# Kernel optimization log

Hardware: AMD Instinct MI355X
Metric: run time of the kernel (lower is better)

Reference implementation:

```python
import jax, jax.numpy as jnp
import numpy as np

N, T, DM = 8192, 32, 128   # nodes, patches, d_model (d_in = T*DM = 4096)
M, NNZ = 1024, 131072      # hyperedges, incidences
EPS = 1e-5
SLOPE = 0.2


def _bn(x, g, b, axes):
    # BatchNorm with batch statistics (training-mode math, eval dropout)
    m = jnp.mean(x, axis=axes, keepdims=True)
    v = jnp.var(x, axis=axes, keepdims=True)
    return (x - m) / jnp.sqrt(v + EPS) * g + b


def _hconv(x, he_attr, he_n, he_e, W, att, bias, heads):
    # PyG HypergraphConv, use_attention=True, attention_mode='node', concat=False
    out = W.shape[1] // heads
    xt = (x @ W).reshape(N, heads, out)          # [N, H, F]
    et = (he_attr @ W).reshape(M, heads, out)    # [M, H, F]
    xi = xt[he_n]                                # [nnz, H, F] gather node feats
    ej = et[he_e]                                # [nnz, H, F] gather edge feats
    alpha = jnp.sum(jnp.concatenate([xi, ej], axis=-1) * att, axis=-1)  # [nnz, H]
    alpha = jax.nn.leaky_relu(alpha, SLOPE)
    # segment softmax grouped by hyperedge (attention_mode='node')
    amax = jax.ops.segment_max(alpha, he_e, num_segments=M)
    ex = jnp.exp(alpha - amax[he_e])
    alpha = ex / jax.ops.segment_sum(ex, he_e, num_segments=M)[he_e]
    # degree normalizers (hyperedge_weight == 1)
    ones = jnp.ones((NNZ,), x.dtype)
    Dn = jax.ops.segment_sum(ones, he_n, num_segments=N)
    Dinv = jnp.where(Dn > 0, 1.0 / Dn, 0.0)
    Bm = jax.ops.segment_sum(ones, he_e, num_segments=M)
    Binv = jnp.where(Bm > 0, 1.0 / Bm, 0.0)
    # node -> edge, then edge -> node message passing
    eo = jax.ops.segment_sum(alpha[:, :, None] * Binv[he_e][:, None, None] * xi,
                             he_e, num_segments=M)                     # [M, H, F]
    no = jax.ops.segment_sum(alpha[:, :, None] * Dinv[he_n][:, None, None] * eo[he_e],
                             he_n, num_segments=N)                     # [N, H, F]
    return no.mean(axis=1) + bias  # concat=False -> mean over heads


def setup_inputs() -> dict:
    key = jax.random.key(0)
    ks = jax.random.split(key, 16)
    d_in = T * DM
    s = 0.02
    inp = {
        "x": jax.random.normal(ks[0], (N, T, DM), jnp.float32),
        "he_nodes": jax.random.randint(ks[1], (NNZ,), 0, N),
        "he_edges": jax.random.randint(ks[2], (NNZ,), 0, M),
        "W1": jax.random.normal(ks[3], (d_in, DM), jnp.float32) * s,
        "b1": jnp.zeros((DM,), jnp.float32),
        "g1": jnp.ones((DM,), jnp.float32), "be1": jnp.zeros((DM,), jnp.float32),
        "Wh1": jax.random.normal(ks[4], (DM, 4 * DM), jnp.float32) * s,
        "att1": jax.random.normal(ks[5], (1, 4, 2 * DM), jnp.float32) * s,
        "bh1": jnp.zeros((DM,), jnp.float32),
        "g2": jnp.ones((DM,), jnp.float32), "be2": jnp.zeros((DM,), jnp.float32),
        "Wh2": jax.random.normal(ks[6], (DM, DM), jnp.float32) * s,
        "att2": jax.random.normal(ks[7], (1, 1, 2 * DM), jnp.float32) * s,
        "bh2": jnp.zeros((DM,), jnp.float32),
        "g3": jnp.ones((DM,), jnp.float32), "be3": jnp.zeros((DM,), jnp.float32),
        "W3": jax.random.normal(ks[8], (DM, d_in), jnp.float32) * s,
        "b3": jnp.zeros((d_in,), jnp.float32),
        "g4": jnp.ones((DM,), jnp.float32), "be4": jnp.zeros((DM,), jnp.float32),
    }
    return inp


def reference(x, he_nodes, he_edges, W1, b1, g1, be1, Wh1, att1, bh1,
              g2, be2, Wh2, att2, bh2, g3, be3, W3, b3, g4, be4):
    src = x
    h = x.reshape(N, T * DM)
    h = jax.nn.leaky_relu(h @ W1 + b1, SLOPE)
    h = _bn(h, g1, be1, 0)
    # hyperedge_attr = incidence^T @ h  (== to_dense_adj(...).T @ h)
    he_attr = jax.ops.segment_sum(h[he_nodes], he_edges, num_segments=M)
    h = h + _hconv(h, he_attr, he_nodes, he_edges, Wh1, att1, bh1, 4)
    h = _bn(h, g2, be2, 0)
    he_attr = jax.ops.segment_sum(h[he_nodes], he_edges, num_segments=M)
    h = h + _hconv(h, he_attr, he_nodes, he_edges, Wh2, att2, bh2, 1)
    h = _bn(h, g3, be3, 0)
    h = jax.nn.leaky_relu(h @ W3 + b3, SLOPE)
    h = src + h.reshape(N, T, DM)
    h = _bn(h, g4, be4, (0, 1))  # BN over channel DM, stats over (N, T)
    return h
```

## Files before the change

kernel.cpp:

```cpp
#include <hip/hip_runtime.h>
#include <hip/hip_bf16.h>
#include <math.h>

#define NN   8192
#define TT   32
#define DIN  4096
#define MME  1024
#define NNZK 131072
#define EPSV 1e-5f
#define MALL (NN + MME)
#define NSLOT 8

typedef __attribute__((ext_vector_type(8))) short bf16x8;
typedef __attribute__((ext_vector_type(4))) float f32x4;

__device__ __forceinline__ float lrelu(float v){ return v > 0.f ? v : 0.2f*v; }
__device__ __forceinline__ short f2b(float f){
    union { __hip_bfloat16 h; short s; } u; u.h = __float2bfloat16(f); return u.s;
}
__device__ __forceinline__ float b2f(short s){
    union { float f; unsigned u; } u; u.u = ((unsigned)(unsigned short)s) << 16; return u.f;
}

__global__ void zero_i(int* p, int n){ int i = blockIdx.x*256 + threadIdx.x; if (i < n) p[i] = 0; }
__global__ void zero_f(float* p, int n){ int i = blockIdx.x*256 + threadIdx.x; if (i < n) p[i] = 0.f; }

__global__ void count_seg(const int* __restrict__ he_n, const int* __restrict__ he_e,
                          int* __restrict__ ncnt, int* __restrict__ ecnt){
    int k = blockIdx.x*256 + threadIdx.x;
    if (k < NNZK){ atomicAdd(&ecnt[he_e[k]], 1); atomicAdd(&ncnt[he_n[k]], 1); }
}

__device__ void scan_body(const int* __restrict__ cnt, int* __restrict__ off,
                          int* __restrict__ cur, int n){
    int t = threadIdx.x;
    int lane = t & 63, wv = t >> 6;
    int chunk = n >> 10;
    int base = t*chunk;
    int s = 0;
#pragma unroll 4
    for (int i = 0; i < chunk; i++) s += cnt[base+i];
    int v = s;
    for (int d = 1; d < 64; d <<= 1){
        int u = __shfl_up(v, d);
        if (lane >= d) v += u;
    }
    __shared__ int wsum[16];
    if (lane == 63) wsum[wv] = v;
    __syncthreads();
    if (wv == 0 && lane < 16){
        int w2 = wsum[lane];
        for (int d = 1; d < 16; d <<= 1){
            int u = __shfl_up(w2, d);
            if (lane >= d) w2 += u;
        }
        wsum[lane] = w2;
    }
    __syncthreads();
    int excl = v - s + (wv > 0 ? wsum[wv-1] : 0);
    for (int i = 0; i < chunk; i++){
        off[base+i] = excl;
        cur[base+i] = excl;
        excl += cnt[base+i];
    }
    if (t == 1023) off[n] = excl;
}

__global__ void scan2(const int* ecnt, int* eoffb, int* ecur,
                      const int* ncnt, int* noffb, int* ncur){
    if (blockIdx.x == 0) scan_body(ecnt, eoffb, ecur, MME);
    else                 scan_body(ncnt, noffb, ncur, NN);
}

__global__ void fill_both(const int* __restrict__ he_n, const int* __restrict__ he_e,
                          int* __restrict__ ecur, int* __restrict__ ncur,
                          int* __restrict__ eperm, int* __restrict__ enode,
                          int* __restrict__ nperm, int* __restrict__ nedge){
    int k = blockIdx.x*256 + threadIdx.x;
    if (k < NNZK){
        int e = he_e[k], n = he_n[k];
        int p = atomicAdd(&ecur[e], 1); eperm[p] = k; enode[p] = n;
        int q = atomicAdd(&ncur[n], 1); nperm[q] = k; nedge[q] = e;
    }
}

__global__ __launch_bounds__(256) void convert_x(const float4* __restrict__ x,
                                                 bf16x8* __restrict__ xb, int n8){
    int stride = gridDim.x*256;
    for (int i = blockIdx.x*256 + threadIdx.x; i < n8; i += stride){
        float4 lo = x[2*i], hi = x[2*i+1];
        bf16x8 v;
        v[0]=f2b(lo.x); v[1]=f2b(lo.y); v[2]=f2b(lo.z); v[3]=f2b(lo.w);
        v[4]=f2b(hi.x); v[5]=f2b(hi.y); v[6]=f2b(hi.z); v[7]=f2b(hi.w);
        xb[i] = v;
    }
}

__device__ void wconv_body(const float* __restrict__ W, __hip_bfloat16* __restrict__ BT,
                           int K, int N, int gx, int gy){
    __shared__ float tile[32][33];
    int k0 = gy*32, n0 = gx*32;
    int tx = threadIdx.x & 31, ty = threadIdx.x >> 5;
    for (int i = ty; i < 32; i += 8) tile[i][tx] = W[(size_t)(k0+i)*N + n0+tx];
    __syncthreads();
    for (int i = ty; i < 32; i += 8)
        BT[(size_t)(n0+i)*K + k0 + tx] = __float2bfloat16(tile[tx][i]);
}

__global__ void wconv_all(const float* W1, __hip_bfloat16* W1T,
                          const float* Wh1, __hip_bfloat16* Wh1T,
                          const float* Wh2, __hip_bfloat16* Wh2T,
                          const float* W3, __hip_bfloat16* W3T){
    int b = blockIdx.x;
    if (b < 512)            wconv_body(W1,  W1T,  DIN, 128, b % 4,          b / 4);
    else if (b < 576){ b -= 512; wconv_body(Wh1, Wh1T, 128, 512, b % 16, b / 16); }
    else if (b < 592){ b -= 576; wconv_body(Wh2, Wh2T, 128, 128, b % 4,  b / 4); }
    else             { b -= 592; wconv_body(W3,  W3T,  128, DIN, b % 128, b / 128); }
}

#define SWZ(b) ((b) ^ ((((b) >> 6) & 7) << 4))

__global__ __launch_bounds__(256) void gemm_bb(
    const __hip_bfloat16* __restrict__ Ab, const __hip_bfloat16* __restrict__ Bwt,
    __hip_bfloat16* __restrict__ Cb, int M, int N, int K, int kchunk)
{
    __shared__ f32x4 WsRaw[512];
    __shared__ f32x4 XsRaw[512];
    char* Ws = (char*)WsRaw;
    char* Xs = (char*)XsRaw;
    const int tid = threadIdx.x;
    const int lane = tid & 63;
    const int w = tid >> 6;
    const int m0 = blockIdx.y << 7, n0 = blockIdx.x << 7;
    const int kz = blockIdx.z * kchunk;
    const int wN = (w >> 1) << 6, wM = (w & 1) << 6;

    const int s0 = tid, s1 = tid + 256;
    const int r0 = s0 >> 2, k0b = (s0 & 3) << 3;
    const int r1 = s1 >> 2, k1b = (s1 & 3) << 3;
    const __hip_bfloat16* pA0 = Ab + (size_t)(m0 + r0)*K + kz + k0b;
    const __hip_bfloat16* pA1 = Ab + (size_t)(m0 + r1)*K + kz + k1b;
    const __hip_bfloat16* pW0 = Bwt + (size_t)(n0 + r0)*K + kz + k0b;
    const __hip_bfloat16* pW1 = Bwt + (size_t)(n0 + r1)*K + kz + k1b;
    const int wo0 = SWZ(s0 << 4), wo1 = SWZ(s1 << 4);

    int rwOff[4], rxOff[4];
#pragma unroll
    for (int f = 0; f < 4; f++){
        rwOff[f] = SWZ((wN + f*16 + (lane & 15))*64 + ((lane >> 4) << 4));
        rxOff[f] = SWZ((wM + f*16 + (lane & 15))*64 + ((lane >> 4) << 4));
// ... 121 lines not shown
    const int ncb = wN + ((lane >> 4) << 2);
    if (tid < 128) sAx[tid] = 0.f;
    __syncthreads();
    const int h = blockIdx.x;
    const int aoff = (m0 >= NN) ? 128 : 0;
    const float* av = attv + h*256 + aoff;
    float4 a4[4];
#pragma unroll
    for (int i = 0; i < 4; i++) a4[i] = *(const float4*)&av[ncb + i*16];
    float sj[4] = {0.f, 0.f, 0.f, 0.f};
#pragma unroll
    for (int j = 0; j < 4; j++){
        int row = m0 + mc + j*16;
#pragma unroll
        for (int i = 0; i < 4; i++){
            int col = n0 + ncb + i*16;
            f32x4 v = acc[i][j];
            short4 sv = { f2b(v[0]), f2b(v[1]), f2b(v[2]), f2b(v[3]) };
            *(short4*)&Cb[(size_t)row*N + col] = sv;
            sj[j] += v[0]*a4[i].x + v[1]*a4[i].y + v[2]*a4[i].z + v[3]*a4[i].w;
        }
    }
#pragma unroll
    for (int j = 0; j < 4; j++) atomicAdd(&sAx[mc + j*16], sj[j]);
    __syncthreads();
    if (tid < 128){
        int row = m0 + tid;
        float val = sAx[tid];
        if (row < NN) axo[row*H + h] = val;
        else          aeo[(row - NN)*H + h] = val;
    }
}

__global__ __launch_bounds__(256) void gemm_nt7(
    const float* __restrict__ Aact, const __hip_bfloat16* __restrict__ Bwt,
    __hip_bfloat16* __restrict__ Cb, const float* __restrict__ bias,
    const float* __restrict__ coefA, int M, int N, int K)
{
    __shared__ f32x4 WsRaw[512];
    __shared__ f32x4 XsRaw[512];
    char* Ws = (char*)WsRaw;
    char* Xs = (char*)XsRaw;
    const int tid = threadIdx.x;
    const int lane = tid & 63;
    const int w = tid >> 6;
    const int m0 = blockIdx.y << 7, n0 = blockIdx.x << 7;
    const int wN = (w >> 1) << 6, wM = (w & 1) << 6;

    const int s0 = tid, s1 = tid + 256;
    const int r0 = s0 >> 2, k0b = (s0 & 3) << 3;
    const int r1 = s1 >> 2, k1b = (s1 & 3) << 3;
    const float* pX0 = Aact + (size_t)(m0 + r0)*K + k0b;
    const float* pX1 = Aact + (size_t)(m0 + r1)*K + k1b;
    const __hip_bfloat16* pW0 = Bwt + (size_t)(n0 + r0)*K + k0b;
    const __hip_bfloat16* pW1 = Bwt + (size_t)(n0 + r1)*K + k1b;
    const int wo0 = SWZ(s0 << 4), wo1 = SWZ(s1 << 4);

    int rwOff[4], rxOff[4];
#pragma unroll
    for (int f = 0; f < 4; f++){
        rwOff[f] = SWZ((wN + f*16 + (lane & 15))*64 + ((lane >> 4) << 4));
        rxOff[f] = SWZ((wM + f*16 + (lane & 15))*64 + ((lane >> 4) << 4));
    }

    f32x4 acc[4][4] = {};

    float4 x0l = *(const float4*)pX0, x0h = *(const float4*)(pX0+4);
    float4 x1l = *(const float4*)pX1, x1h = *(const float4*)(pX1+4);
    bf16x8 w0 = *(const bf16x8*)pW0, w1 = *(const bf16x8*)pW1;

// ... 22 lines not shown
        *(bf16x8*)(Xs + wo1) = vx1;
        *(bf16x8*)(Ws + wo0) = w0;
        *(bf16x8*)(Ws + wo1) = w1;
        __syncthreads();
        if (ks + 1 < nsteps){
            pX0 += 32; pX1 += 32; pW0 += 32; pW1 += 32;
            x0l = *(const float4*)pX0; x0h = *(const float4*)(pX0+4);
            x1l = *(const float4*)pX1; x1h = *(const float4*)(pX1+4);
            w0 = *(const bf16x8*)pW0;  w1 = *(const bf16x8*)pW1;
        }
        bf16x8 wf[4], xf[4];
#pragma unroll
        for (int f = 0; f < 4; f++){
            wf[f] = *(const bf16x8*)(Ws + rwOff[f]);
            xf[f] = *(const bf16x8*)(Xs + rxOff[f]);
        }
#pragma unroll
        for (int i = 0; i < 4; i++)
#pragma unroll
            for (int j = 0; j < 4; j++)
                acc[i][j] = __builtin_amdgcn_mfma_f32_16x16x32_bf16(wf[i], xf[j], acc[i][j], 0, 0, 0);
    }

    const int mc = wM + (lane & 15);
    const int ncb = wN + ((lane >> 4) << 2);
#pragma unroll
    for (int j = 0; j < 4; j++){
        int row = m0 + mc + j*16;
#pragma unroll
        for (int i = 0; i < 4; i++){
            int col = n0 + ncb + i*16;
            f32x4 v = acc[i][j];
            float4 b4 = *(const float4*)&bias[col];
            short4 sv = { f2b(lrelu(v[0] + b4.x)), f2b(lrelu(v[1] + b4.y)),
                          f2b(lrelu(v[2] + b4.z)), f2b(lrelu(v[3] + b4.w)) };
            *(short4*)&Cb[(size_t)row*N + col] = sv;
        }
    }
}

__global__ void reduce8s(const __hip_bfloat16* __restrict__ part, const float* __restrict__ bias,
                         float* __restrict__ out, int nf4, int parts, float* __restrict__ slots){
    int tid = threadIdx.x;
    int i = blockIdx.x*256 + tid;
    const short4* p4 = (const short4*)part;
    short4 v0 = p4[i];
    float4 s = { b2f(v0.x), b2f(v0.y), b2f(v0.z), b2f(v0.w) };
    for (int z = 1; z < parts; z++){
        short4 p = p4[(size_t)z*nf4 + i];
        s.x += b2f(p.x); s.y += b2f(p.y); s.z += b2f(p.z); s.w += b2f(p.w);
    }
    int c0 = (i & 31) << 2;
    s.x = lrelu(s.x + bias[c0+0]); s.y = lrelu(s.y + bias[c0+1]);
    s.z = lrelu(s.z + bias[c0+2]); s.w = lrelu(s.w + bias[c0+3]);
    ((float4*)out)[i] = s;
    __shared__ float S[128], Q[128];
    if (tid < 128){ S[tid] = 0.f; Q[tid] = 0.f; }
    __syncthreads();
    atomicAdd(&S[c0+0], s.x); atomicAdd(&Q[c0+0], s.x*s.x);
    atomicAdd(&S[c0+1], s.y); atomicAdd(&Q[c0+1], s.y*s.y);
    atomicAdd(&S[c0+2], s.z); atomicAdd(&Q[c0+2], s.z*s.z);
    atomicAdd(&S[c0+3], s.w); atomicAdd(&Q[c0+3], s.w*s.w);
    __syncthreads();
    if (tid < 128){
        int slot = blockIdx.x & (NSLOT-1);
        atomicAdd(&slots[slot*256 + tid], S[tid]);
        atomicAdd(&slots[slot*256 + 128 + tid], Q[tid]);
    }
}

__global__ __launch_bounds__(256) void final_stats(
    const bf16x8* __restrict__ xb, const bf16x8* __restrict__ f,
    float* __restrict__ slots, int n8)
{
    int tid = threadIdx.x;
    float s[8] = {0,0,0,0,0,0,0,0}, q[8] = {0,0,0,0,0,0,0,0};
    int stride = gridDim.x*256;
    for (int i = blockIdx.x*256 + tid; i < n8; i += stride){
        bf16x8 xv = xb[i], fv = f[i];
#pragma unroll
        for (int j = 0; j < 8; j++){
            float y = b2f(xv[j]) + b2f(fv[j]);
            s[j] += y; q[j] += y*y;
        }
    }
    __shared__ float S[128], Q[128];
    if (tid < 128){ S[tid] = 0.f; Q[tid] = 0.f; }
    __syncthreads();
    int c0 = (tid & 15) << 3;
#pragma unroll
    for (int j = 0; j < 8; j++){
        atomicAdd(&S[c0+j], s[j]);
        atomicAdd(&Q[c0+j], q[j]);
    }
    __syncthreads();
    if (tid < 128){
        int slot = blockIdx.x & (NSLOT-1);
        atomicAdd(&slots[slot*256 + tid], S[tid]);
        atomicAdd(&slots[slot*256 + 128 + tid], Q[tid]);
    }
}

__global__ __launch_bounds__(256) void final_apply(
    const bf16x8* __restrict__ xb, const bf16x8* __restrict__ f,
    const float* __restrict__ coef, float4* __restrict__ out, int n8)
{
    int tid = threadIdx.x;
    int c0 = (tid & 15) << 3;
    float sc[8], sh[8];
#pragma unroll
    for (int j = 0; j < 8; j++){ sc[j] = coef[c0+j]; sh[j] = coef[128+c0+j]; }
    int stride = gridDim.x*256;
    for (int i = blockIdx.x*256 + tid; i < n8; i += stride){
        bf16x8 xv = xb[i], fv = f[i];
        float4 lo, hi;
        lo.x = (b2f(xv[0]) + b2f(fv[0]))*sc[0] + sh[0];
        lo.y = (b2f(xv[1]) + b2f(fv[1]))*sc[1] + sh[1];
        lo.z = (b2f(xv[2]) + b2f(fv[2]))*sc[2] + sh[2];
        lo.w = (b2f(xv[3]) + b2f(fv[3]))*sc[3] + sh[3];
        hi.x = (b2f(xv[4]) + b2f(fv[4]))*sc[4] + sh[4];
        hi.y = (b2f(xv[5]) + b2f(fv[5]))*sc[5] + sh[5];
        hi.z = (b2f(xv[6]) + b2f(fv[6]))*sc[6] + sh[6];
        hi.w = (b2f(xv[7]) + b2f(fv[7]))*sc[7] + sh[7];
        out[2*i]   = lo;
        out[2*i+1] = hi;
    }
}

__global__ void bn_stats_v2(const float* __restrict__ x, float* __restrict__ slots, int rows){
    int cg = threadIdx.x & 31, rg = threadIdx.x >> 5;
    float4 s = {0,0,0,0}, q = {0,0,0,0};
    for (int r = blockIdx.x*8 + rg; r < rows; r += gridDim.x*8){
        float4 v = ((const float4*)x)[(size_t)r*32 + cg];
        s.x += v.x; q.x += v.x*v.x;
        s.y += v.y; q.y += v.y*v.y;
        s.z += v.z; q.z += v.z*v.z;
        s.w += v.w; q.w += v.w*v.w;
    }
    __shared__ float S[128], Q[128];
    if (threadIdx.x < 128){ S[threadIdx.x] = 0.f; Q[threadIdx.x] = 0.f; }
    __syncthreads();
    int c0 = cg << 2;
    atomicAdd(&S[c0+0], s.x); atomicAdd(&Q[c0+0], q.x);
    atomicAdd(&S[c0+1], s.y); atomicAdd(&Q[c0+1], q.y);
    atomicAdd(&S[c0+2], s.z); atomicAdd(&Q[c0+2], q.z);
    atomicAdd(&S[c0+3], s.w); atomicAdd(&Q[c0+3], q.w);
    __syncthreads();
    if (threadIdx.x < 128){
        int slot = blockIdx.x & (NSLOT-1);
        atomicAdd(&slots[slot*256 + threadIdx.x], S[threadIdx.x]);
        atomicAdd(&slots[slot*256 + 128 + threadIdx.x], Q[threadIdx.x]);
    }
}

__global__ void bn_finalize2z(float* __restrict__ slots, int nslots,
                              const float* __restrict__ g, const float* __restrict__ b,
                              float invR, float* __restrict__ coef){
    int c = threadIdx.x;
    float s = 0.f, q = 0.f;
    for (int k = 0; k < nslots; k++){
        s += slots[k*256 + c]; q += slots[k*256 + 128 + c];
        slots[k*256 + c] = 0.f; slots[k*256 + 128 + c] = 0.f;
    }
    float m = s*invR;
    float v = q*invR - m*m;
    float sc = g[c]*rsqrtf(v + EPSV);
    coef[c] = sc;
    coef[128 + c] = b[c] - m*sc;
}

__global__ void bn_apply4(float4* __restrict__ x, const float* __restrict__ coef, size_t n4){
    size_t i = (size_t)blockIdx.x*blockDim.x + threadIdx.x;
    size_t stride = (size_t)gridDim.x*blockDim.x;
    for (; i < n4; i += stride){
        int c0 = (int)(i & 31) * 4;
        float4 v = x[i];
        v.x = v.x*coef[c0+0] + coef[128+c0+0];
        v.y = v.y*coef[c0+1] + coef[128+c0+1];
        v.z = v.z*coef[c0+2] + coef[128+c0+2];
        v.w = v.w*coef[c0+3] + coef[128+c0+3];
        x[i] = v;
    }
}

__global__ void seg_sum_edge(const int* __restrict__ eoff, const int* __restrict__ enode,
                             const float* __restrict__ h, float* __restrict__ out){
    int m = blockIdx.x, t = threadIdx.x;
    int jg = t >> 5, cq = t & 31;
    int s0 = eoff[m], cnt = eoff[m+1] - s0;
    __shared__ int sn[128];
    __shared__ float4 comb[4][32];
    float4 acc = {0,0,0,0};
    for (int base = 0; base < cnt; base += 128){
        int i = base + t;
        if (i < cnt) sn[t] = enode[s0+i];
        __syncthreads();
        int lim = min(128, cnt - base);
        for (int j = jg; j < lim; j += 4){
            float4 v = *(const float4*)&h[(size_t)sn[j]*128 + cq*4];
            acc.x += v.x; acc.y += v.y; acc.z += v.z; acc.w += v.w;
        }
        __syncthreads();
    }
    comb[jg][cq] = acc;
    __syncthreads();
    if (t < 32){
        float4 a = comb[0][t], b = comb[1][t], c = comb[2][t], d = comb[3][t];
        float4 tot = { a.x+b.x+c.x+d.x, a.y+b.y+c.y+d.y, a.z+b.z+c.z+d.z, a.w+b.w+c.w+d.w };
        *(float4*)&out[(size_t)m*128 + t*4] = tot;
    }
}

template<int H>
__global__ void seg_softmax(const int* __restrict__ eoff, const int* __restrict__ eperm,
                            const int* __restrict__ enode,
                            const float* __restrict__ ax, const float* __restrict__ ae,
                            float* __restrict__ alpha){
    int m = blockIdx.x, t = threadIdx.x;
    int s0 = eoff[m], cnt = eoff[m+1] - s0;
    if (cnt == 0) return;
    __shared__ float red[128];
    float aeh[H];
#pragma unroll
    for (int h = 0; h < H; h++) aeh[h] = ae[m*H + h];
    float lmax[H];
#pragma unroll
    for (int h = 0; h < H; h++) lmax[h] = -1e30f;
    for (int i = t; i < cnt; i += 128){
        int k = eperm[s0+i]; int n = enode[s0+i];
#pragma unroll
        for (int h = 0; h < H; h++){
            float v = lrelu(ax[n*H + h] + aeh[h]);
            alpha[(size_t)k*H + h] = v;
            lmax[h] = fmaxf(lmax[h], v);
        }
    }
    float gmax[H];
#pragma unroll
    for (int h = 0; h < H; h++){
        red[t] = lmax[h]; __syncthreads();
        for (int s = 64; s > 0; s >>= 1){ if (t < s) red[t] = fmaxf(red[t], red[t+s]); __syncthreads(); }
        gmax[h] = red[0]; __syncthreads();
    }
    float lsum[H];
#pragma unroll
    for (int h = 0; h < H; h++) lsum[h] = 0.f;
    for (int i = t; i < cnt; i += 128){
        int k = eperm[s0+i];
#pragma unroll
        for (int h = 0; h < H; h++){
            float ex = __expf(alpha[(size_t)k*H + h] - gmax[h]);
            alpha[(size_t)k*H + h] = ex;
            lsum[h] += ex;
        }
    }
    float ginv[H];
#pragma unroll
    for (int h = 0; h < H; h++){
        red[t] = lsum[h]; __syncthreads();
        for (int s = 64; s > 0; s >>= 1){ if (t < s) red[t] += red[t+s]; __syncthreads(); }
        ginv[h] = 1.f/red[0]; __syncthreads();
    }
    for (int i = t; i < cnt; i += 128){
        int k = eperm[s0+i];
#pragma unroll
        for (int h = 0; h < H; h++) alpha[(size_t)k*H + h] *= ginv[h];
    }
}

__global__ void seg_eo4(const int* __restrict__ eoff, const int* __restrict__ eperm,
                        const int* __restrict__ enode,
                        const float* __restrict__ alpha, const __hip_bfloat16* __restrict__ xt,
                        float* __restrict__ eo){
    int m = blockIdx.x, t = threadIdx.x;
    int jpar = t >> 7, cq = t & 127;
    int hq = cq >> 5;
    int s0 = eoff[m], cnt = eoff[m+1] - s0;
    __shared__ int sn[128];
    __shared__ float sa[128][4];
    __shared__ float comb[256][4];
    float acc[4] = {0.f, 0.f, 0.f, 0.f};
    for (int base = 0; base < cnt; base += 128){
        int i = base + t;
        if (t < 128 && i < cnt){
            sn[t] = enode[s0+i];
            *(float4*)sa[t] = *(const float4*)&alpha[(size_t)eperm[s0+i]*4];
        }
        __syncthreads();
        int lim = min(128, cnt - base);
        for (int j = jpar; j < lim; j += 2){
            const ushort* p = (const ushort*)xt + (size_t)sn[j]*512 + cq*4;
            ushort4 u = *(const ushort4*)p;
            float a = sa[j][hq];
            acc[0] += a*b2f((short)u.x); acc[1] += a*b2f((short)u.y);
            acc[2] += a*b2f((short)u.z); acc[3] += a*b2f((short)u.w);
        }
        __syncthreads();
    }
    comb[t][0] = acc[0]; comb[t][1] = acc[1]; comb[t][2] = acc[2]; comb[t][3] = acc[3];
    __syncthreads();
    if (t < 128){
        float binv = cnt > 0 ? 1.f/(float)cnt : 0.f;
#pragma unroll
        for (int i2 = 0; i2 < 4; i2++){
            int ch = t*4 + i2;
            int h = ch >> 7, c = ch & 127;
            eo[(size_t)m*512 + c*4 + h] = (comb[t][i2] + comb[t+128][i2]) * binv;
        }
    }
}

__global__ void seg_eo1b(const int* __restrict__ eoff, const int* __restrict__ eperm,
                         const int* __restrict__ enode,
                         const float* __restrict__ alpha, const __hip_bfloat16* __restrict__ xt,
                         float* __restrict__ eo){
    int m = blockIdx.x, t = threadIdx.x;
    int jg = t >> 5, cq = t & 31;
    int s0 = eoff[m], cnt = eoff[m+1] - s0;
    __shared__ int sn[128];
    __shared__ float sa[128];
    __shared__ float4 comb[4][32];
    float4 acc = {0,0,0,0};
    for (int base = 0; base < cnt; base += 128){
        int i = base + t;
        if (i < cnt){
            sn[t] = enode[s0+i];
            sa[t] = alpha[eperm[s0+i]];
        }
        __syncthreads();
        int lim = min(128, cnt - base);
        for (int j = jg; j < lim; j += 4){
            const ushort* p = (const ushort*)xt + (size_t)sn[j]*128 + cq*4;
            ushort4 u = *(const ushort4*)p;
            float a = sa[j];
            acc.x += a*b2f((short)u.x); acc.y += a*b2f((short)u.y);
            acc.z += a*b2f((short)u.z); acc.w += a*b2f((short)u.w);
        }
        __syncthreads();
    }
    comb[jg][cq] = acc;
    __syncthreads();
    if (t < 32){
        float binv = cnt > 0 ? 1.f/(float)cnt : 0.f;
        float4 a = comb[0][t], b = comb[1][t], c = comb[2][t], d = comb[3][t];
        float4 tot = { (a.x+b.x+c.x+d.x)*binv, (a.y+b.y+c.y+d.y)*binv,
                       (a.z+b.z+c.z+d.z)*binv, (a.w+b.w+c.w+d.w)*binv };
        *(float4*)&eo[(size_t)m*128 + t*4] = tot;
    }
}

__global__ void seg_node_out4(const int* __restrict__ noff, const int* __restrict__ nperm,
                              const int* __restrict__ nedge,
                              const float* __restrict__ alpha, const float* __restrict__ eo,
                              const float* __restrict__ hin, const float* __restrict__ bias,
                              float* __restrict__ hout){
    int n = blockIdx.x, c = threadIdx.x;
    int s0 = noff[n], cnt = noff[n+1] - s0;
    float acc = 0.f;
    for (int i = 0; i < cnt; i++){
        int k = nperm[s0+i]; int e = nedge[s0+i];
        float4 al = *(const float4*)&alpha[(size_t)k*4];
        float4 ev = *(const float4*)&eo[(size_t)e*512 + c*4];
        acc += al.x*ev.x + al.y*ev.y + al.z*ev.z + al.w*ev.w;
    }
    float dinv = cnt > 0 ? 1.f/((float)cnt*4.f) : 0.f;
    hout[(size_t)n*128 + c] = hin[(size_t)n*128 + c] + bias[c] + acc*dinv;
}

__global__ void seg_node_out1(const int* __restrict__ noff, const int* __restrict__ nperm,
                              const int* __restrict__ nedge,
                              const float* __restrict__ alpha, const float* __restrict__ eo,
                              const float* __restrict__ hin, const float* __restrict__ bias,
                              float* __restrict__ hout){
    int n = blockIdx.x, c = threadIdx.x;
    int s0 = noff[n], cnt = noff[n+1] - s0;
    float acc = 0.f;
// ... 6 lines not shown
}

extern "C" void kernel_launch(void* const* d_in, const int* in_sizes, int n_in,
                              void* d_out, int out_size, void* d_ws, size_t ws_size,
                              hipStream_t stream){
    const float* x    = (const float*)d_in[0];
    const int*   he_n = (const int*)  d_in[1];
    const int*   he_e = (const int*)  d_in[2];
    const float* W1   = (const float*)d_in[3];
    const float* b1   = (const float*)d_in[4];
    const float* g1   = (const float*)d_in[5];
    const float* be1  = (const float*)d_in[6];
    const float* Wh1  = (const float*)d_in[7];
    const float* att1 = (const float*)d_in[8];
    const float* bh1  = (const float*)d_in[9];
    const float* g2   = (const float*)d_in[10];
    const float* be2  = (const float*)d_in[11];
    const float* Wh2  = (const float*)d_in[12];
    const float* att2 = (const float*)d_in[13];
    const float* bh2  = (const float*)d_in[14];
    const float* g3   = (const float*)d_in[15];
    const float* be3  = (const float*)d_in[16];
    const float* W3   = (const float*)d_in[17];
    const float* b3   = (const float*)d_in[18];
    const float* g4   = (const float*)d_in[19];
    const float* be4  = (const float*)d_in[20];
    float* out = (float*)d_out;

    char* ws = (char*)d_ws;
    size_t off = 0;
    auto alloc = [&](size_t bytes)->char*{ char* p = ws + off; off += (bytes + 255) & ~(size_t)255; return p; };

    char* big = alloc((size_t)NN*DIN*2);
    __hip_bfloat16* fbuf = (__hip_bfloat16*)big;
    __hip_bfloat16* part = (__hip_bfloat16*)big;
    __hip_bfloat16* xt1b = (__hip_bfloat16*)(big + (size_t)16*NN*128*2);
    __hip_bfloat16* xbuf = (__hip_bfloat16*)alloc((size_t)NN*DIN*2);

    float* hall1  = (float*)alloc((size_t)MALL*128*4);
    float* hall2  = (float*)alloc((size_t)MALL*128*4);
    float* h3     = (float*)alloc((size_t)NN*128*4);
    __hip_bfloat16* xt2b = (__hip_bfloat16*)alloc((size_t)MALL*128*2);
    float* eo     = (float*)alloc((size_t)MME*512*4);
    float* alpha  = (float*)alloc((size_t)NNZK*4*4);
    float* ax     = (float*)alloc((size_t)NN*4*4);
    float* ae     = (float*)alloc((size_t)MME*4*4);
    float* slots  = (float*)alloc((size_t)NSLOT*256*4);
    float* coef   = (float*)alloc(256*4);
    __hip_bfloat16* W1T  = (__hip_bfloat16*)alloc((size_t)128*DIN*2);
    __hip_bfloat16* Wh1T = (__hip_bfloat16*)alloc((size_t)512*128*2);
    __hip_bfloat16* Wh2T = (__hip_bfloat16*)alloc((size_t)128*128*2);
    __hip_bfloat16* W3T  = (__hip_bfloat16*)alloc((size_t)DIN*128*2);
    int* ecnt  = (int*)alloc(MME*4);
    int* ncnt  = (int*)alloc(NN*4);
    int* eoffb = (int*)alloc((MME+1)*4);
    int* ecur  = (int*)alloc(MME*4);
    int* noffb = (int*)alloc((NN+1)*4);
    int* ncur  = (int*)alloc(NN*4);
    int* eperm = (int*)alloc((size_t)NNZK*4);
    int* nperm = (int*)alloc((size_t)NNZK*4);
    int* enode = (int*)alloc((size_t)NNZK*4);
    int* nedge = (int*)alloc((size_t)NNZK*4);

    convert_x<<<2048, 256, 0, stream>>>((const float4*)x, (bf16x8*)xbuf, NN*DIN/8);

    zero_i<<<(MME+NN+255)/256, 256, 0, stream>>>(ecnt, MME+NN);
    count_seg<<<NNZK/256, 256, 0, stream>>>(he_n, he_e, ncnt, ecnt);
    scan2<<<2, 1024, 0, stream>>>(ecnt, eoffb, ecur, ncnt, noffb, ncur);
    fill_both<<<NNZK/256, 256, 0, stream>>>(he_n, he_e, ecur, ncur, eperm, enode, nperm, nedge);

    wconv_all<<<1104, 256, 0, stream>>>(W1, W1T, Wh1, Wh1T, Wh2, Wh2T, W3, W3T);

    gemm_bb<<<dim3(1, NN/128, 16), 256, 0, stream>>>(xbuf, W1T, part, NN, 128, DIN, DIN/16);
    zero_f<<<NSLOT, 256, 0, stream>>>(slots, NSLOT*256);
    reduce8s<<<NN*128/4/256, 256, 0, stream>>>(part, b1, hall1, NN*128/4, 16, slots);
    bn_finalize2z<<<1, 128, 0, stream>>>(slots, NSLOT, g1, be1, 1.f/NN, coef);
    bn_apply4<<<1024, 256, 0, stream>>>((float4*)hall1, coef, (size_t)NN*32);

    seg_sum_edge<<<MME, 128, 0, stream>>>(eoffb, enode, hall1, hall1 + (size_t)NN*128);
    gemm_att<4><<<dim3(4, MALL/128), 256, 0, stream>>>(hall1, Wh1T, xt1b, att1, ax, ae, MALL, 512, 128);
    seg_softmax<4><<<MME, 128, 0, stream>>>(eoffb, eperm, enode, ax, ae, alpha);
    seg_eo4<<<MME, 256, 0, stream>>>(eoffb, eperm, enode, alpha, xt1b, eo);
    seg_node_out4<<<NN, 128, 0, stream>>>(noffb, nperm, nedge, alpha, eo, hall1, bh1, hall2);
    bn_stats_v2<<<256, 256, 0, stream>>>(hall2, slots, NN);
    bn_finalize2z<<<1, 128, 0, stream>>>(slots, NSLOT, g2, be2, 1.f/NN, coef);
    bn_apply4<<<1024, 256, 0, stream>>>((float4*)hall2, coef, (size_t)NN*32);

    seg_sum_edge<<<MME, 128, 0, stream>>>(eoffb, enode, hall2, hall2 + (size_t)NN*128);
    gemm_att<1><<<dim3(1, MALL/128), 256, 0, stream>>>(hall2, Wh2T, xt2b, att2, ax, ae, MALL, 128, 128);
    seg_softmax<1><<<MME, 128, 0, stream>>>(eoffb, eperm, enode, ax, ae, alpha);
    seg_eo1b<<<MME, 128, 0, stream>>>(eoffb, eperm, enode, alpha, xt2b, eo);
    seg_node_out1<<<NN, 128, 0, stream>>>(noffb, nperm, nedge, alpha, eo, hall2, bh2, h3);

    bn_stats_v2<<<256, 256, 0, stream>>>(h3, slots, NN);
    bn_finalize2z<<<1, 128, 0, stream>>>(slots, NSLOT, g3, be3, 1.f/NN, coef);

    gemm_nt7<<<dim3(DIN/128, NN/128), 256, 0, stream>>>(h3, W3T, fbuf, b3, coef, NN, DIN, 128);
    final_stats<<<2048, 256, 0, stream>>>((const bf16x8*)xbuf, (const bf16x8*)fbuf, slots, NN*DIN/8);
    bn_finalize2z<<<1, 128, 0, stream>>>(slots, NSLOT, g4, be4, 1.f/((float)NN*TT), coef);
    final_apply<<<2048, 256, 0, stream>>>((const bf16x8*)xbuf, (const bf16x8*)fbuf, coef, (float4*)out, NN*DIN/8);
}
```

Before: 490.0 us.

## Fuse setup kernels, BN finalize tails, softmax+edge aggregation, and residual into GEMM

Merges the x conversion, segment counting and weight transposes into one setup kernel, and merges all zeroing into one kernel. BatchNorm finalization now runs in the last block to arrive, using a ticket counter, which removes separate single-block launches. Segment softmax is fused with the edge aggregation. The residual add is folded into the final GEMM epilogue, so the last stats and apply passes read one bf16 tensor instead of two. The trade-offs are extra atomics and fences, and the residual sum is now rounded to bf16 before the stats are taken.

```diff
diff --git a/kernel.cpp b/kernel.cpp
--- a/kernel.cpp
+++ b/kernel.cpp
@@ -22,13 +22,43 @@
     union { float f; unsigned u; } u; u.u = ((unsigned)(unsigned short)s) << 16; return u.f;
 }
 
-__global__ void zero_i(int* p, int n){ int i = blockIdx.x*256 + threadIdx.x; if (i < n) p[i] = 0; }
-__global__ void zero_f(float* p, int n){ int i = blockIdx.x*256 + threadIdx.x; if (i < n) p[i] = 0.f; }
-
-__global__ void count_seg(const int* __restrict__ he_n, const int* __restrict__ he_e,
-                          int* __restrict__ ncnt, int* __restrict__ ecnt){
-    int k = blockIdx.x*256 + threadIdx.x;
-    if (k < NNZK){ atomicAdd(&ecnt[he_e[k]], 1); atomicAdd(&ncnt[he_n[k]], 1); }
+__global__ void zero_all(int* __restrict__ cnt, int n1, float* __restrict__ slots, int n2,
+                         int* __restrict__ tick, int n3){
+    int i = blockIdx.x*256 + threadIdx.x;
+    if (i < n1) cnt[i] = 0;
+    int j = i - n1;
+    if (j >= 0 && j < n2) slots[j] = 0.f;
+    int k = j - n2;
+    if (k >= 0 && k < n3) tick[k] = 0;
+}
+
+__device__ void finalize_tail(float* __restrict__ slots, int* __restrict__ ticket, int nblocks,
+                              const float* __restrict__ g, const float* __restrict__ b,
+                              float invR, float* __restrict__ coef){
+    __shared__ int isLast;
+    __threadfence();
+    if (threadIdx.x == 0){
+        int old = atomicAdd(ticket, 1);
+        isLast = (old == nblocks - 1) ? 1 : 0;
+    }
+    __syncthreads();
+    if (isLast){
+        __threadfence();
+        if (threadIdx.x < 128){
+            int c = threadIdx.x;
+            float s = 0.f, q = 0.f;
+            for (int k = 0; k < NSLOT; k++){
+                s += slots[k*256 + c]; q += slots[k*256 + 128 + c];
+                slots[k*256 + c] = 0.f; slots[k*256 + 128 + c] = 0.f;
+            }
+            float m = s*invR;
+            float v = q*invR - m*m;
+            float sc = g[c]*rsqrtf(v + EPSV);
+            coef[c] = sc;
+            coef[128 + c] = b[c] - m*sc;
+            if (c == 0) *ticket = 0;
+        }
+    }
 }
 
 __device__ void scan_body(const int* __restrict__ cnt, int* __restrict__ off,
@@ -84,18 +114,6 @@
     }
 }
 
-__global__ __launch_bounds__(256) void convert_x(const float4* __restrict__ x,
-                                                 bf16x8* __restrict__ xb, int n8){
-    int stride = gridDim.x*256;
-    for (int i = blockIdx.x*256 + threadIdx.x; i < n8; i += stride){
-        float4 lo = x[2*i], hi = x[2*i+1];
-        bf16x8 v;
-        v[0]=f2b(lo.x); v[1]=f2b(lo.y); v[2]=f2b(lo.z); v[3]=f2b(lo.w);
-        v[4]=f2b(hi.x); v[5]=f2b(hi.y); v[6]=f2b(hi.z); v[7]=f2b(hi.w);
-        xb[i] = v;
-    }
-}
-
 __device__ void wconv_body(const float* __restrict__ W, __hip_bfloat16* __restrict__ BT,
                            int K, int N, int gx, int gy){
     __shared__ float tile[32][33];
@@ -107,15 +125,33 @@
         BT[(size_t)(n0+i)*K + k0 + tx] = __float2bfloat16(tile[tx][i]);
 }
 
-__global__ void wconv_all(const float* W1, __hip_bfloat16* W1T,
-                          const float* Wh1, __hip_bfloat16* Wh1T,
-                          const float* Wh2, __hip_bfloat16* Wh2T,
-                          const float* W3, __hip_bfloat16* W3T){
+__global__ __launch_bounds__(256) void setup_all(
+    const float4* __restrict__ x, bf16x8* __restrict__ xb,
+    const int* __restrict__ he_n, const int* __restrict__ he_e,
+    int* __restrict__ ncnt, int* __restrict__ ecnt,
+    const float* W1, __hip_bfloat16* W1T, const float* Wh1, __hip_bfloat16* Wh1T,
+    const float* Wh2, __hip_bfloat16* Wh2T, const float* W3, __hip_bfloat16* W3T)
+{
     int b = blockIdx.x;
-    if (b < 512)            wconv_body(W1,  W1T,  DIN, 128, b % 4,          b / 4);
-    else if (b < 576){ b -= 512; wconv_body(Wh1, Wh1T, 128, 512, b % 16, b / 16); }
-    else if (b < 592){ b -= 576; wconv_body(Wh2, Wh2T, 128, 128, b % 4,  b / 4); }
-    else             { b -= 592; wconv_body(W3,  W3T,  128, DIN, b % 128, b / 128); }
+    if (b < 2048){
+        const int n8 = NN*DIN/8;
+        for (int i = b*256 + threadIdx.x; i < n8; i += 2048*256){
+            float4 lo = x[2*i], hi = x[2*i+1];
+            bf16x8 v;
+            v[0]=f2b(lo.x); v[1]=f2b(lo.y); v[2]=f2b(lo.z); v[3]=f2b(lo.w);
+            v[4]=f2b(hi.x); v[5]=f2b(hi.y); v[6]=f2b(hi.z); v[7]=f2b(hi.w);
+            xb[i] = v;
+        }
+    } else if (b < 2560){
+        int k = (b - 2048)*256 + threadIdx.x;
+        if (k < NNZK){ atomicAdd(&ecnt[he_e[k]], 1); atomicAdd(&ncnt[he_n[k]], 1); }
+    } else {
+        int c = b - 2560;
+        if (c < 512)            wconv_body(W1,  W1T,  DIN, 128, c % 4,   c / 4);
+        else if (c < 576){ c -= 512; wconv_body(Wh1, Wh1T, 128, 512, c % 16, c / 16); }
+        else if (c < 592){ c -= 576; wconv_body(Wh2, Wh2T, 128, 128, c % 4,  c / 4); }
+        else             { c -= 592; wconv_body(W3,  W3T,  128, DIN, c % 128, c / 128); }
+    }
 }
 
 #define SWZ(b) ((b) ^ ((((b) >> 6) & 7) << 4))
@@ -303,10 +339,10 @@
     }
 }
 
-__global__ __launch_bounds__(256) void gemm_nt7(
+__global__ __launch_bounds__(256) void gemm_nt8(
     const float* __restrict__ Aact, const __hip_bfloat16* __restrict__ Bwt,
-    __hip_bfloat16* __restrict__ Cb, const float* __restrict__ bias,
-    const float* __restrict__ coefA, int M, int N, int K)
+    const __hip_bfloat16* __restrict__ xb, __hip_bfloat16* __restrict__ Yb,
+    const float* __restrict__ bias, const float* __restrict__ coefA, int M, int N, int K)
 {
     __shared__ f32x4 WsRaw[512];
     __shared__ f32x4 XsRaw[512];
@@ -395,15 +431,20 @@
             int col = n0 + ncb + i*16;
             f32x4 v = acc[i][j];
             float4 b4 = *(const float4*)&bias[col];
-            short4 sv = { f2b(lrelu(v[0] + b4.x)), f2b(lrelu(v[1] + b4.y)),
-                          f2b(lrelu(v[2] + b4.z)), f2b(lrelu(v[3] + b4.w)) };
-            *(short4*)&Cb[(size_t)row*N + col] = sv;
-        }
-    }
-}
-
-__global__ void reduce8s(const __hip_bfloat16* __restrict__ part, const float* __restrict__ bias,
-                         float* __restrict__ out, int nf4, int parts, float* __restrict__ slots){
+            short4 xv = *(const short4*)&xb[(size_t)row*N + col];
+            short4 sv = { f2b(lrelu(v[0] + b4.x) + b2f(xv.x)),
+                          f2b(lrelu(v[1] + b4.y) + b2f(xv.y)),
+                          f2b(lrelu(v[2] + b4.z) + b2f(xv.z)),
+                          f2b(lrelu(v[3] + b4.w) + b2f(xv.w)) };
+            *(short4*)&Yb[(size_t)row*N + col] = sv;
+        }
+    }
+}
+
+__global__ void reduce8s_f(const __hip_bfloat16* __restrict__ part, const float* __restrict__ bias,
+                           float* __restrict__ out, int nf4, int parts, float* __restrict__ slots,
+                           int* __restrict__ ticket, const float* __restrict__ g,
+                           const float* __restrict__ b, float invR, float* __restrict__ coef){
     int tid = threadIdx.x;
     int i = blockIdx.x*256 + tid;
     const short4* p4 = (const short4*)part;
@@ -430,67 +471,12 @@
         atomicAdd(&slots[slot*256 + tid], S[tid]);
         atomicAdd(&slots[slot*256 + 128 + tid], Q[tid]);
     }
-}
-
-__global__ __launch_bounds__(256) void final_stats(
-    const bf16x8* __restrict__ xb, const bf16x8* __restrict__ f,
-    float* __restrict__ slots, int n8)
-{
-    int tid = threadIdx.x;
-    float s[8] = {0,0,0,0,0,0,0,0}, q[8] = {0,0,0,0,0,0,0,0};
-    int stride = gridDim.x*256;
-    for (int i = blockIdx.x*256 + tid; i < n8; i += stride){
-        bf16x8 xv = xb[i], fv = f[i];
-#pragma unroll
-        for (int j = 0; j < 8; j++){
-            float y = b2f(xv[j]) + b2f(fv[j]);
-            s[j] += y; q[j] += y*y;
-        }
-    }
-    __shared__ float S[128], Q[128];
-    if (tid < 128){ S[tid] = 0.f; Q[tid] = 0.f; }
-    __syncthreads();
-    int c0 = (tid & 15) << 3;
-#pragma unroll
-    for (int j = 0; j < 8; j++){
-        atomicAdd(&S[c0+j], s[j]);
-        atomicAdd(&Q[c0+j], q[j]);
-    }
-    __syncthreads();
-    if (tid < 128){
-        int slot = blockIdx.x & (NSLOT-1);
-        atomicAdd(&slots[slot*256 + tid], S[tid]);
-        atomicAdd(&slots[slot*256 + 128 + tid], Q[tid]);
-    }
-}
-
-__global__ __launch_bounds__(256) void final_apply(
-    const bf16x8* __restrict__ xb, const bf16x8* __restrict__ f,
-    const float* __restrict__ coef, float4* __restrict__ out, int n8)
-{
-    int tid = threadIdx.x;
-    int c0 = (tid & 15) << 3;
-    float sc[8], sh[8];
-#pragma unroll
-    for (int j = 0; j < 8; j++){ sc[j] = coef[c0+j]; sh[j] = coef[128+c0+j]; }
-    int stride = gridDim.x*256;
-    for (int i = blockIdx.x*256 + tid; i < n8; i += stride){
-        bf16x8 xv = xb[i], fv = f[i];
-        float4 lo, hi;
-        lo.x = (b2f(xv[0]) + b2f(fv[0]))*sc[0] + sh[0];
-        lo.y = (b2f(xv[1]) + b2f(fv[1]))*sc[1] + sh[1];
-        lo.z = (b2f(xv[2]) + b2f(fv[2]))*sc[2] + sh[2];
-        lo.w = (b2f(xv[3]) + b2f(fv[3]))*sc[3] + sh[3];
-        hi.x = (b2f(xv[4]) + b2f(fv[4]))*sc[4] + sh[4];
-        hi.y = (b2f(xv[5]) + b2f(fv[5]))*sc[5] + sh[5];
-        hi.z = (b2f(xv[6]) + b2f(fv[6]))*sc[6] + sh[6];
-        hi.w = (b2f(xv[7]) + b2f(fv[7]))*sc[7] + sh[7];
-        out[2*i]   = lo;
-        out[2*i+1] = hi;
-    }
-}
-
-__global__ void bn_stats_v2(const float* __restrict__ x, float* __restrict__ slots, int rows){
+    finalize_tail(slots, ticket, gridDim.x, g, b, invR, coef);
+}
+
+__global__ void bn_stats_f(const float* __restrict__ x, float* __restrict__ slots, int rows,
+                           int* __restrict__ ticket, const float* __restrict__ g,
+                           const float* __restrict__ b, float invR, float* __restrict__ coef){
     int cg = threadIdx.x & 31, rg = threadIdx.x >> 5;
     float4 s = {0,0,0,0}, q = {0,0,0,0};
     for (int r = blockIdx.x*8 + rg; r < rows; r += gridDim.x*8){
@@ -514,22 +500,7 @@
         atomicAdd(&slots[slot*256 + threadIdx.x], S[threadIdx.x]);
         atomicAdd(&slots[slot*256 + 128 + threadIdx.x], Q[threadIdx.x]);
     }
-}
-
-__global__ void bn_finalize2z(float* __restrict__ slots, int nslots,
-                              const float* __restrict__ g, const float* __restrict__ b,
-                              float invR, float* __restrict__ coef){
-    int c = threadIdx.x;
-    float s = 0.f, q = 0.f;
-    for (int k = 0; k < nslots; k++){
-        s += slots[k*256 + c]; q += slots[k*256 + 128 + c];
-        slots[k*256 + c] = 0.f; slots[k*256 + 128 + c] = 0.f;
-    }
-    float m = s*invR;
-    float v = q*invR - m*m;
-    float sc = g[c]*rsqrtf(v + EPSV);
-    coef[c] = sc;
-    coef[128 + c] = b[c] - m*sc;
+    finalize_tail(slots, ticket, gridDim.x, g, b, invR, coef);
 }
 
 __global__ void bn_apply4(float4* __restrict__ x, const float* __restrict__ coef, size_t n4){
@@ -546,6 +517,66 @@
     }
 }
 
+__global__ __launch_bounds__(256) void final_stats2(
+    const bf16x8* __restrict__ yb, float* __restrict__ slots, int n8,
+    int* __restrict__ ticket, const float* __restrict__ g,
+    const float* __restrict__ b, float invR, float* __restrict__ coef)
+{
+    int tid = threadIdx.x;
+    float s[8] = {0,0,0,0,0,0,0,0}, q[8] = {0,0,0,0,0,0,0,0};
+    int stride = gridDim.x*256;
+    for (int i = blockIdx.x*256 + tid; i < n8; i += stride){
+        bf16x8 yv = yb[i];
+#pragma unroll
+        for (int j = 0; j < 8; j++){
+            float y = b2f(yv[j]);
+            s[j] += y; q[j] += y*y;
+        }
+    }
+    __shared__ float S[128], Q[128];
+    if (tid < 128){ S[tid] = 0.f; Q[tid] = 0.f; }
+    __syncthreads();
+    int c0 = (tid & 15) << 3;
+#pragma unroll
+    for (int j = 0; j < 8; j++){
+        atomicAdd(&S[c0+j], s[j]);
+        atomicAdd(&Q[c0+j], q[j]);
+    }
+    __syncthreads();
+    if (tid < 128){
+        int slot = blockIdx.x & (NSLOT-1);
+        atomicAdd(&slots[slot*256 + tid], S[tid]);
+        atomicAdd(&slots[slot*256 + 128 + tid], Q[tid]);
+    }
+    finalize_tail(slots, ticket, gridDim.x, g, b, invR, coef);
+}
+
+__global__ __launch_bounds__(256) void final_apply2(
+    const bf16x8* __restrict__ yb, const float* __restrict__ coef,
+    float4* __restrict__ out, int n8)
+{
+    int tid = threadIdx.x;
+    int c0 = (tid & 15) << 3;
+    float sc[8], sh[8];
+#pragma unroll
+    for (int j = 0; j < 8; j++){ sc[j] = coef[c0+j]; sh[j] = coef[128+c0+j]; }
+    int stride = gridDim.x*256;
+    for (int i = blockIdx.x*256 + tid; i < n8; i += stride){
+        bf16x8 yv = yb[i];
+        float4 lo, hi;
+        lo.x = b2f(yv[0])*sc[0] + sh[0];
+        lo.y = b2f(yv[1])*sc[1] + sh[1];
+        lo.z = b2f(yv[2])*sc[2] + sh[2];
+        lo.w = b2f(yv[3])*sc[3] + sh[3];
+        hi.x = b2f(yv[4])*sc[4] + sh[4];
+        hi.y = b2f(yv[5])*sc[5] + sh[5];
+        hi.z = b2f(yv[6])*sc[6] + sh[6];
+        hi.w = b2f(yv[7])*sc[7] + sh[7];
+        out[2*i]   = lo;
+        out[2*i+1] = hi;
+    }
+}
+
 __global__ void seg_sum_edge(const int* __restrict__ eoff, const int* __restrict__ enode,
                              const float* __restrict__ h, float* __restrict__ out){
     int m = blockIdx.x, t = threadIdx.x;
@@ -574,71 +605,63 @@
     }
 }
 
-template<int H>
-__global__ void seg_softmax(const int* __restrict__ eoff, const int* __restrict__ eperm,
-                            const int* __restrict__ enode,
-                            const float* __restrict__ ax, const float* __restrict__ ae,
-                            float* __restrict__ alpha){
+__global__ void seg_soft_eo4(const int* __restrict__ eoff, const int* __restrict__ eperm,
+                             const int* __restrict__ enode,
+                             const float* __restrict__ ax, const float* __restrict__ ae,
+                             float* __restrict__ alpha, const __hip_bfloat16* __restrict__ xt,
+                             float* __restrict__ eo){
     int m = blockIdx.x, t = threadIdx.x;
     int s0 = eoff[m], cnt = eoff[m+1] - s0;
-    if (cnt == 0) return;
-    __shared__ float red[128];
-    float aeh[H];
-#pragma unroll
-    for (int h = 0; h < H; h++) aeh[h] = ae[m*H + h];
-    float lmax[H];
-#pragma unroll
-    for (int h = 0; h < H; h++) lmax[h] = -1e30f;
-    for (int i = t; i < cnt; i += 128){
+    __shared__ float red[256];
+    if (cnt == 0){
+        if (t < 128) *(float4*)&eo[(size_t)m*512 + t*4] = (float4){0,0,0,0};
+        return;
+    }
+    float aeh[4];
+#pragma unroll
+    for (int h = 0; h < 4; h++) aeh[h] = ae[m*4 + h];
+    float lmax[4] = {-1e30f, -1e30f, -1e30f, -1e30f};
+    for (int i = t; i < cnt; i += 256){
         int k = eperm[s0+i]; int n = enode[s0+i];
 #pragma unroll
-        for (int h = 0; h < H; h++){
-            float v = lrelu(ax[n*H + h] + aeh[h]);
-            alpha[(size_t)k*H + h] = v;
+        for (int h = 0; h < 4; h++){
+            float v = lrelu(ax[n*4 + h] + aeh[h]);
+            alpha[(size_t)k*4 + h] = v;
             lmax[h] = fmaxf(lmax[h], v);
         }
     }
-    float gmax[H];
-#pragma unroll
-    for (int h = 0; h < H; h++){
+    float gmax[4];
+#pragma unroll
+    for (int h = 0; h < 4; h++){
         red[t] = lmax[h]; __syncthreads();
-        for (int s = 64; s > 0; s >>= 1){ if (t < s) red[t] = fmaxf(red[t], red[t+s]); __syncthreads(); }
+        for (int s = 128; s > 0; s >>= 1){ if (t < s) red[t] = fmaxf(red[t], red[t+s]); __syncthreads(); }
         gmax[h] = red[0]; __syncthreads();
     }
-    float lsum[H];
-#pragma unroll
-    for (int h = 0; h < H; h++) lsum[h] = 0.f;
-    for (int i = t; i < cnt; i += 128){
+    float lsum[4] = {0.f, 0.f, 0.f, 0.f};
+    for (int i = t; i < cnt; i += 256){
         int k = eperm[s0+i];
 #pragma unroll
-        for (int h = 0; h < H; h++){
-            float ex = __expf(alpha[(size_t)k*H + h] - gmax[h]);
-            alpha[(size_t)k*H + h] = ex;
+        for (int h = 0; h < 4; h++){
+            float ex = __expf(alpha[(size_t)k*4 + h] - gmax[h]);
+            alpha[(size_t)k*4 + h] = ex;
             lsum[h] += ex;
         }
     }
-    float ginv[H];
-#pragma unroll
-    for (int h = 0; h < H; h++){
+    float ginv[4];
+#pragma unroll
+    for (int h = 0; h < 4; h++){
         red[t] = lsum[h]; __syncthreads();
-        for (int s = 64; s > 0; s >>= 1){ if (t < s) red[t] += red[t+s]; __syncthreads(); }
+        for (int s = 128; s > 0; s >>= 1){ if (t < s) red[t] += red[t+s]; __syncthreads(); }
         ginv[h] = 1.f/red[0]; __syncthreads();
     }
-    for (int i = t; i < cnt; i += 128){
+    for (int i = t; i < cnt; i += 256){
         int k = eperm[s0+i];
 #pragma unroll
-        for (int h = 0; h < H; h++) alpha[(size_t)k*H + h] *= ginv[h];
-    }
-}
-
-__global__ void seg_eo4(const int* __restrict__ eoff, const int* __restrict__ eperm,
-                        const int* __restrict__ enode,
-                        const float* __restrict__ alpha, const __hip_bfloat16* __restrict__ xt,
-                        float* __restrict__ eo){
-    int m = blockIdx.x, t = threadIdx.x;
+        for (int h = 0; h < 4; h++) alpha[(size_t)k*4 + h] *= ginv[h];
+    }
+    __syncthreads();
     int jpar = t >> 7, cq = t & 127;
     int hq = cq >> 5;
-    int s0 = eoff[m], cnt = eoff[m+1] - s0;
     __shared__ int sn[128];
     __shared__ float sa[128][4];
     __shared__ float comb[256][4];
@@ -663,7 +686,7 @@
     comb[t][0] = acc[0]; comb[t][1] = acc[1]; comb[t][2] = acc[2]; comb[t][3] = acc[3];
     __syncthreads();
     if (t < 128){
-        float binv = cnt > 0 ? 1.f/(float)cnt : 0.f;
+        float binv = 1.f/(float)cnt;
 #pragma unroll
         for (int i2 = 0; i2 < 4; i2++){
             int ch = t*4 + i2;
@@ -673,13 +696,45 @@
     }
 }
 
-__global__ void seg_eo1b(const int* __restrict__ eoff, const int* __restrict__ eperm,
-                         const int* __restrict__ enode,
-                         const float* __restrict__ alpha, const __hip_bfloat16* __restrict__ xt,
-                         float* __restrict__ eo){
+__global__ void seg_soft_eo1(const int* __restrict__ eoff, const int* __restrict__ eperm,
+                             const int* __restrict__ enode,
+                             const float* __restrict__ ax, const float* __restrict__ ae,
+                             float* __restrict__ alpha, const __hip_bfloat16* __restrict__ xt,
+                             float* __restrict__ eo){
     int m = blockIdx.x, t = threadIdx.x;
+    int s0 = eoff[m], cnt = eoff[m+1] - s0;
+    __shared__ float red[128];
+    if (cnt == 0){
+        if (t < 32) *(float4*)&eo[(size_t)m*128 + t*4] = (float4){0,0,0,0};
+        return;
+    }
+    float aeh = ae[m];
+    float lmax = -1e30f;
+    for (int i = t; i < cnt; i += 128){
+        int k = eperm[s0+i]; int n = enode[s0+i];
+        float v = lrelu(ax[n] + aeh);
+        alpha[k] = v;
+        lmax = fmaxf(lmax, v);
+    }
+    red[t] = lmax; __syncthreads();
+    for (int s = 64; s > 0; s >>= 1){ if (t < s) red[t] = fmaxf(red[t], red[t+s]); __syncthreads(); }
+    float gmax = red[0]; __syncthreads();
+    float lsum = 0.f;
+    for (int i = t; i < cnt; i += 128){
+        int k = eperm[s0+i];
+        float ex = __expf(alpha[k] - gmax);
+        alpha[k] = ex;
+        lsum += ex;
+    }
+    red[t] = lsum; __syncthreads();
+    for (int s = 64; s > 0; s >>= 1){ if (t < s) red[t] += red[t+s]; __syncthreads(); }
+    float ginv = 1.f/red[0]; __syncthreads();
+    for (int i = t; i < cnt; i += 128){
+        int k = eperm[s0+i];
+        alpha[k] *= ginv;
+    }
+    __syncthreads();
     int jg = t >> 5, cq = t & 31;
-    int s0 = eoff[m], cnt = eoff[m+1] - s0;
     __shared__ int sn[128];
     __shared__ float sa[128];
     __shared__ float4 comb[4][32];
@@ -704,7 +759,7 @@
     comb[jg][cq] = acc;
     __syncthreads();
     if (t < 32){
-        float binv = cnt > 0 ? 1.f/(float)cnt : 0.f;
+        float binv = 1.f/(float)cnt;
         float4 a = comb[0][t], b = comb[1][t], c = comb[2][t], d = comb[3][t];
         float4 tot = { (a.x+b.x+c.x+d.x)*binv, (a.y+b.y+c.y+d.y)*binv,
                        (a.z+b.z+c.z+d.z)*binv, (a.w+b.w+c.w+d.w)*binv };
@@ -777,7 +832,7 @@
     auto alloc = [&](size_t bytes)->char*{ char* p = ws + off; off += (bytes + 255) & ~(size_t)255; return p; };
 
     char* big = alloc((size_t)NN*DIN*2);
-    __hip_bfloat16* fbuf = (__hip_bfloat16*)big;
+    __hip_bfloat16* ybuf = (__hip_bfloat16*)big;
     __hip_bfloat16* part = (__hip_bfloat16*)big;
     __hip_bfloat16* xt1b = (__hip_bfloat16*)(big + (size_t)16*NN*128*2);
     __hip_bfloat16* xbuf = (__hip_bfloat16*)alloc((size_t)NN*DIN*2);
@@ -792,6 +847,7 @@
     float* ae     = (float*)alloc((size_t)MME*4*4);
     float* slots  = (float*)alloc((size_t)NSLOT*256*4);
     float* coef   = (float*)alloc(256*4);
+    int*   tick   = (int*)alloc(16*4);
     __hip_bfloat16* W1T  = (__hip_bfloat16*)alloc((size_t)128*DIN*2);
     __hip_bfloat16* Wh1T = (__hip_bfloat16*)alloc((size_t)512*128*2);
     __hip_bfloat16* Wh2T = (__hip_bfloat16*)alloc((size_t)128*128*2);
@@ -807,41 +863,35 @@
     int* enode = (int*)alloc((size_t)NNZK*4);
     int* nedge = (int*)alloc((size_t)NNZK*4);
 
-    convert_x<<<2048, 256, 0, stream>>>((const float4*)x, (bf16x8*)xbuf, NN*DIN/8);
-
-    zero_i<<<(MME+NN+255)/256, 256, 0, stream>>>(ecnt, MME+NN);
-    count_seg<<<NNZK/256, 256, 0, stream>>>(he_n, he_e, ncnt, ecnt);
+    zero_all<<<(MME+NN+NSLOT*256+16+255)/256, 256, 0, stream>>>(ecnt, MME+NN, slots, NSLOT*256, tick, 16);
+
+    setup_all<<<3664, 256, 0, stream>>>((const float4*)x, (bf16x8*)xbuf, he_n, he_e, ncnt, ecnt,
+                                        W1, W1T, Wh1, Wh1T, Wh2, Wh2T, W3, W3T);
+
     scan2<<<2, 1024, 0, stream>>>(ecnt, eoffb, ecur, ncnt, noffb, ncur);
     fill_both<<<NNZK/256, 256, 0, stream>>>(he_n, he_e, ecur, ncur, eperm, enode, nperm, nedge);
 
-    wconv_all<<<1104, 256, 0, stream>>>(W1, W1T, Wh1, Wh1T, Wh2, Wh2T, W3, W3T);
-
     gemm_bb<<<dim3(1, NN/128, 16), 256, 0, stream>>>(xbuf, W1T, part, NN, 128, DIN, DIN/16);
-    zero_f<<<NSLOT, 256, 0, stream>>>(slots, NSLOT*256);
-    reduce8s<<<NN*128/4/256, 256, 0, stream>>>(part, b1, hall1, NN*128/4, 16, slots);
-    bn_finalize2z<<<1, 128, 0, stream>>>(slots, NSLOT, g1, be1, 1.f/NN, coef);
+    reduce8s_f<<<NN*128/4/256, 256, 0, stream>>>(part, b1, hall1, NN*128/4, 16, slots,
+                                                 &tick[0], g1, be1, 1.f/NN, coef);
     bn_apply4<<<1024, 256, 0, stream>>>((float4*)hall1, coef, (size_t)NN*32);
 
     seg_sum_edge<<<MME, 128, 0, stream>>>(eoffb, enode, hall1, hall1 + (size_t)NN*128);
     gemm_att<4><<<dim3(4, MALL/128), 256, 0, stream>>>(hall1, Wh1T, xt1b, att1, ax, ae, MALL, 512, 128);
-    seg_softmax<4><<<MME, 128, 0, stream>>>(eoffb, eperm, enode, ax, ae, alpha);
-    seg_eo4<<<MME, 256, 0, stream>>>(eoffb, eperm, enode, alpha, xt1b, eo);
+    seg_soft_eo4<<<MME, 256, 0, stream>>>(eoffb, eperm, enode, ax, ae, alpha, xt1b, eo);
     seg_node_out4<<<NN, 128, 0, stream>>>(noffb, nperm, nedge, alpha, eo, hall1, bh1, hall2);
-    bn_stats_v2<<<256, 256, 0, stream>>>(hall2, slots, NN);
-    bn_finalize2z<<<1, 128, 0, stream>>>(slots, NSLOT, g2, be2, 1.f/NN, coef);
+    bn_stats_f<<<256, 256, 0, stream>>>(hall2, slots, NN, &tick[1], g2, be2, 1.f/NN, coef);
     bn_apply4<<<1024, 256, 0, stream>>>((float4*)hall2, coef, (size_t)NN*32);
 
     seg_sum_edge<<<MME, 128, 0, stream>>>(eoffb, enode, hall2, hall2 + (size_t)NN*128);
     gemm_att<1><<<dim3(1, MALL/128), 256, 0, stream>>>(hall2, Wh2T, xt2b, att2, ax, ae, MALL, 128, 128);
-    seg_softmax<1><<<MME, 128, 0, stream>>>(eoffb, eperm, enode, ax, ae, alpha);
-    seg_eo1b<<<MME, 128, 0, stream>>>(eoffb, eperm, enode, alpha, xt2b, eo);
+    seg_soft_eo1<<<MME, 128, 0, stream>>>(eoffb, eperm, enode, ax, ae, alpha, xt2b, eo);
     seg_node_out1<<<NN, 128, 0, stream>>>(noffb, nperm, nedge, alpha, eo, hall2, bh2, h3);
 
-    bn_stats_v2<<<256, 256, 0, stream>>>(h3, slots, NN);
-    bn_finalize2z<<<1, 128, 0, stream>>>(slots, NSLOT, g3, be3, 1.f/NN, coef);
-
-    gemm_nt7<<<dim3(DIN/128, NN/128), 256, 0, stream>>>(h3, W3T, fbuf, b3, coef, NN, DIN, 128);
-    final_stats<<<2048, 256, 0, stream>>>((const bf16x8*)xbuf, (const bf16x8*)fbuf, slots, NN*DIN/8);
-    bn_finalize2z<<<1, 128, 0, stream>>>(slots, NSLOT, g4, be4, 1.f/((float)NN*TT), coef);
-    final_apply<<<2048, 256, 0, stream>>>((const bf16x8*)xbuf, (const bf16x8*)fbuf, coef, (float4*)out, NN*DIN/8);
-}
+    bn_stats_f<<<256, 256, 0, stream>>>(h3, slots, NN, &tick[2], g3, be3, 1.f/NN, coef);
+
+    gemm_nt8<<<dim3(DIN/128, NN/128), 256, 0, stream>>>(h3, W3T, xbuf, ybuf, b3, coef, NN, DIN, 128);
+    final_stats2<<<2048, 256, 0, stream>>>((const bf16x8*)ybuf, slots, NN*DIN/8,
+                                           &tick[3], g4, be4, 1.f/((float)NN*TT), coef);
+    final_apply2<<<2048, 256, 0, stream>>>((const bf16x8*)ybuf, coef, (float4*)out, NN*DIN/8);
+}
```

After: 615.0 us. 1.26x slower.
